# Kernel tuning notes

Measured on AMD Instinct MI355X. Metric: run time of the kernel, lower is better.

Reference implementation:

```python
import jax, jax.numpy as jnp
import numpy as np

DIM = 64
SQRT_DIM = np.sqrt(DIM).astype(np.float32)
NEG_INF = -1e9


def setup_inputs() -> dict:
    key = jax.random.key(0)
    kq, kk, kv, km = jax.random.split(key, 4)
    B, Q, K, D = 32, 1024, 1024, DIM
    query = jax.random.normal(kq, (B, Q, D), dtype=jnp.float32)
    k = jax.random.normal(kk, (B, K, D), dtype=jnp.float32)
    value = jax.random.normal(kv, (B, K, D), dtype=jnp.float32)
    mask = jax.random.randint(km, (B, Q, K), 0, 2).astype(jnp.bool_)
    return {"query": query, "key": k, "value": value, "mask": mask}


def reference(query, key, value, mask):
    # score: [B, Q, K]
    score = jnp.einsum('bqd,bkd->bqk', query, key) / SQRT_DIM
    score = jnp.where(mask, NEG_INF, score)
    attn = jax.nn.softmax(score, axis=-1)
    context = jnp.einsum('bqk,bkd->bqd', attn, value)
    return (context, attn)
```

## Files before the change

kernel.cpp:

```cpp
#include <hip/hip_runtime.h>

constexpr int BATCH = 32;
constexpr int QLEN  = 1024;
constexpr int KLEN  = 1024;
constexpr int DIM   = 64;
constexpr int TQ    = 16;

typedef float    f32x4 __attribute__((ext_vector_type(4)));
typedef int      i32x4 __attribute__((ext_vector_type(4)));
typedef _Float16 f16x8 __attribute__((ext_vector_type(8)));
typedef _Float16 f16x4 __attribute__((ext_vector_type(4)));
typedef unsigned long long u64;
typedef unsigned int u32;
typedef u64 u64x2 __attribute__((ext_vector_type(2)));

__device__ __forceinline__ f16x8 cvt_h8(f32x4 a, f32x4 b) {
  f16x8 h;
  h[0] = (_Float16)a[0]; h[1] = (_Float16)a[1]; h[2] = (_Float16)a[2]; h[3] = (_Float16)a[3];
  h[4] = (_Float16)b[0]; h[5] = (_Float16)b[1]; h[6] = (_Float16)b[2]; h[7] = (_Float16)b[3];
  return h;
}

constexpr int TK = 128;
__global__ __launch_bounds__(256)
void vtkh_kernel(const float* __restrict__ V, const float* __restrict__ Kg,
                 _Float16* __restrict__ Vt, _Float16* __restrict__ Kh) {
  __shared__ _Float16 lt[DIM][TK + 8];
  const int b = blockIdx.y, k0 = blockIdx.x * TK;
  const int t = threadIdx.x;
  const int d4 = (t & 15) * 4;
  #pragma unroll
  for (int p = 0; p < TK / 16; ++p) {
    const int kl = (t >> 4) + p * 16;
    const f32x4 v = *(const f32x4*)(V + ((size_t)(b * KLEN + k0 + kl)) * DIM + d4);
    #pragma unroll
    for (int j = 0; j < 4; ++j) lt[d4 + j][kl] = (_Float16)v[j];
  }
  #pragma unroll
  for (int p = 0; p < 8; ++p) {
    const int idx = t + p * 256;
    const int kl = idx >> 4, dd = (idx & 15) * 4;
    const f32x4 v = *(const f32x4*)(Kg + ((size_t)(b * KLEN + k0 + kl)) * DIM + dd);
    f16x4 h = { (_Float16)v[0], (_Float16)v[1], (_Float16)v[2], (_Float16)v[3] };
    *(f16x4*)(Kh + ((size_t)(b * KLEN + k0 + kl)) * DIM + dd) = h;
  }
  __syncthreads();
  const int d = t >> 2;
  #pragma unroll
  for (int j2 = 0; j2 < TK / 32; ++j2) {
    const int seg = (t & 3) + j2 * 4;
    *(f16x8*)(Vt + (size_t)b * DIM * KLEN + (size_t)d * KLEN + k0 + seg * 8) =
        *(const f16x8*)(&lt[d][seg * 8]);
  }
}

__global__ __launch_bounds__(256)
void maskpack_kernel(const int* __restrict__ Mg, u64* __restrict__ Mp) {
  const int l  = threadIdx.x & 63;
  const int gw = blockIdx.x * 4 + (threadIdx.x >> 6);
  for (int row = gw; row < BATCH * QLEN; row += 8192) {
    const int* mr = Mg + (size_t)row * KLEN;
    u64 myw = 0;
    #pragma unroll
    for (int c = 0; c < 4; ++c) {
      const i32x4 v = __builtin_nontemporal_load((const i32x4*)(mr + c * 256 + l * 4));
      #pragma unroll
      for (int u = 0; u < 4; ++u) {
        const u64 bl = __ballot(v[u] != 0);
        if (l == c * 4 + u) myw = bl;
      }
    }
    if (l < 16) Mp[(size_t)row * 16 + l] = myw;
  }
}

__global__ __launch_bounds__(64)
void sdpa_kernel(const float* __restrict__ Qg, const _Float16* __restrict__ Kh,
                 const _Float16* __restrict__ Vt, const u64* __restrict__ Mp,
                 float* __restrict__ Ctx, float* __restrict__ Attn)
{
  const int l    = threadIdx.x;
  const int n16  = l & 15;
  const int quad = l >> 4;

  const int lin  = blockIdx.x;
  const int nlin = (lin & 7) * (BATCH * (QLEN / TQ) / 8) + (lin >> 3);
  const int b    = nlin >> 6;
  const int q0   = (nlin & 63) * TQ;

  const float* qb = Qg + ((size_t)(b * QLEN + q0 + n16)) * DIM + quad * 8;
  f32x4 qa0 = *(const f32x4*)(qb),      qa1 = *(const f32x4*)(qb + 4);
  f32x4 qa2 = *(const f32x4*)(qb + 32), qa3 = *(const f32x4*)(qb + 36);
  #pragma unroll
  for (int i = 0; i < 4; ++i) { qa0[i] *= 0.125f; qa1[i] *= 0.125f; qa2[i] *= 0.125f; qa3[i] *= 0.125f; }
  const f16x8 aq0 = cvt_h8(qa0, qa1);
  const f16x8 aq1 = cvt_h8(qa2, qa3);

  const _Float16* kb_base = Kh + (size_t)b * KLEN * DIM + quad * 8;
  const u64* mrow = Mp + ((size_t)(b * QLEN + q0 + n16)) * 16;

  float rsum = 0.f;
  #pragma unroll
  for (int g = 0; g < 4; ++g) {
    const u64x2 w01 = *(const u64x2*)(mrow + g * 4);
    const u64x2 w23 = *(const u64x2*)(mrow + g * 4 + 2);
    const u64 w[4] = { w01[0], w01[1], w23[0], w23[1] };
    #pragma unroll
    for (int tt = 0; tt < 16; ++tt) {
      const int t = g * 16 + tt;
      const _Float16* kp = kb_base + (size_t)(t * 16 + n16) * DIM;
      const f16x8 ak0 = *(const f16x8*)(kp);
      const f16x8 ak1 = *(const f16x8*)(kp + 32);
      f32x4 acc = {0.f, 0.f, 0.f, 0.f};
      acc = __builtin_amdgcn_mfma_f32_16x16x32_f16(ak0, aq0, acc, 0, 0, 0);
      acc = __builtin_amdgcn_mfma_f32_16x16x32_f16(ak1, aq1, acc, 0, 0, 0);
      const u32 sh = tt * 4 + quad;
      #pragma unroll
      for (int i = 0; i < 4; ++i)
        rsum += ((w[i] >> sh) & 1ULL) ? 0.f : __expf(acc[i]);
    }
  }
  rsum += __shfl_xor(rsum, 16, 64);
  rsum += __shfl_xor(rsum, 32, 64);
  const float inv = __builtin_amdgcn_rcpf(rsum);

  float* arow = Attn + ((size_t)(b * QLEN + q0 + n16)) * KLEN;
  const _Float16* vtb = Vt + (size_t)b * DIM * KLEN;
  f32x4 cacc[4] = { {0.f,0.f,0.f,0.f}, {0.f,0.f,0.f,0.f}, {0.f,0.f,0.f,0.f}, {0.f,0.f,0.f,0.f} };
  #pragma unroll
  for (int g = 0; g < 4; ++g) {
    const u64x2 w01 = *(const u64x2*)(mrow + g * 4);
    const u64x2 w23 = *(const u64x2*)(mrow + g * 4 + 2);
    const u64 w[4] = { w01[0], w01[1], w23[0], w23[1] };
    #pragma unroll
    for (int m = 0; m < 8; ++m) {
      uint2 pw[2];
      #pragma unroll
      for (int h = 0; h < 2; ++h) {
        const int t = g * 16 + m * 2 + h;
        const _Float16* kp = kb_base + (size_t)(t * 16 + n16) * DIM;
        const f16x8 ak0 = *(const f16x8*)(kp);
        const f16x8 ak1 = *(const f16x8*)(kp + 32);
        f32x4 acc = {0.f, 0.f, 0.f, 0.f};
        acc = __builtin_amdgcn_mfma_f32_16x16x32_f16(ak0, aq0, acc, 0, 0, 0);
        acc = __builtin_amdgcn_mfma_f32_16x16x32_f16(ak1, aq1, acc, 0, 0, 0);
        const u32 sh = (t & 15) * 4 + quad;
        f32x4 e;
        #pragma unroll
        for (int i = 0; i < 4; ++i)
          e[i] = ((w[i] >> sh) & 1ULL) ? 0.f : __expf(acc[i]) * inv;
        *(f32x4*)(arow + t * 16 + quad * 4) = e;
        f16x4 ph = { (_Float16)e[0], (_Float16)e[1], (_Float16)e[2], (_Float16)e[3] };
        __builtin_memcpy(&pw[h], &ph, 8);
      }
      const int s0 = n16 + ((quad & 1) << 5);
      const u32 x0a = (u32)__shfl((int)pw[0].x, s0, 64);
      const u32 y0a = (u32)__shfl((int)pw[0].y, s0, 64);
      const u32 x1a = (u32)__shfl((int)pw[1].x, s0, 64);
      const u32 y1a = (u32)__shfl((int)pw[1].y, s0, 64);
      const u32 x0b = (u32)__shfl((int)pw[0].x, s0 + 16, 64);
      const u32 y0b = (u32)__shfl((int)pw[0].y, s0 + 16, 64);
      const u32 x1b = (u32)__shfl((int)pw[1].x, s0 + 16, 64);
      const u32 y1b = (u32)__shfl((int)pw[1].y, s0 + 16, 64);
      const bool hs = (quad & 2) != 0;
      const u32 dd[4] = { hs ? x1a : x0a, hs ? y1a : y0a,
                          hs ? x1b : x0b, hs ? y1b : y0b };
      f16x8 pa; __builtin_memcpy(&pa, dd, 16);
      const int K0 = g * 256 + m * 32;
      #pragma unroll
      for (int dt = 0; dt < 4; ++dt) {
        const f16x8 bv = *(const f16x8*)(vtb + (size_t)(dt * 16 + n16) * KLEN + K0 + quad * 8);
        cacc[dt] = __builtin_amdgcn_mfma_f32_16x16x32_f16(pa, bv, cacc[dt], 0, 0, 0);
      }
    }
  }
  #pragma unroll
  for (int dt = 0; dt < 4; ++dt)
    #pragma unroll
    for (int i = 0; i < 4; ++i)
      Ctx[((size_t)(b * QLEN + q0 + quad * 4 + i)) * DIM + dt * 16 + n16] = cacc[dt][i];
}

extern "C" void kernel_launch(void* const* d_in, const int* in_sizes, int n_in,
                              void* d_out, int out_size, void* d_ws, size_t ws_size,
                              hipStream_t stream) {
  const float* Qg = (const float*)d_in[0];
  const float* Kg = (const float*)d_in[1];
  const float* Vg = (const float*)d_in[2];
  const int*   Mg = (const int*)d_in[3];
  float* Ctx  = (float*)d_out;
  float* Attn = (float*)d_out + (size_t)BATCH * QLEN * DIM;
  _Float16* Vt = (_Float16*)d_ws;
  u64* Mp = (u64*)((char*)d_ws + (size_t)BATCH * DIM * KLEN * 2);
  _Float16* Kh = (_Float16*)((char*)d_ws + (size_t)BATCH * DIM * KLEN * 2 +
                             (size_t)BATCH * QLEN * 16 * 8);

  dim3 tgrid(KLEN / TK, BATCH);
  vtkh_kernel<<<tgrid, 256, 0, stream>>>(Vg, Kg, Vt, Kh);

  maskpack_kernel<<<2048, 256, 0, stream>>>(Mg, Mp);

  sdpa_kernel<<<2048, 64, 0, stream>>>(Qg, Kh, Vt, Mp, Ctx, Attn);
}
```

Before: 332.2 us.

## Fuse mask read into attention kernel and split key range across four waves

Removes the separate mask-packing kernel, so the attention kernel reads the int mask directly. Each block now has four waves, each handling a quarter of the keys. Row sums are combined through shared memory, and context partials are reduced in LDS before the store. Exponentials are cached as fp16 from the first pass, so QK is not recomputed, and exp2 with a log2e-folded scale replaces expf. The trade-off is more LDS use, two block barriers and fp16 rounding of the cached exponentials before the attention output is written.

```diff
diff --git a/kernel.cpp b/kernel.cpp
--- a/kernel.cpp
+++ b/kernel.cpp
@@ -12,7 +12,6 @@
 typedef _Float16 f16x4 __attribute__((ext_vector_type(4)));
 typedef unsigned long long u64;
 typedef unsigned int u32;
-typedef u64 u64x2 __attribute__((ext_vector_type(2)));
 
 __device__ __forceinline__ f16x8 cvt_h8(f32x4 a, f32x4 b) {
   f16x8 h;
@@ -54,32 +53,17 @@
   }
 }
 
-__global__ __launch_bounds__(256)
-void maskpack_kernel(const int* __restrict__ Mg, u64* __restrict__ Mp) {
-  const int l  = threadIdx.x & 63;
-  const int gw = blockIdx.x * 4 + (threadIdx.x >> 6);
-  for (int row = gw; row < BATCH * QLEN; row += 8192) {
-    const int* mr = Mg + (size_t)row * KLEN;
-    u64 myw = 0;
-    #pragma unroll
-    for (int c = 0; c < 4; ++c) {
-      const i32x4 v = __builtin_nontemporal_load((const i32x4*)(mr + c * 256 + l * 4));
-      #pragma unroll
-      for (int u = 0; u < 4; ++u) {
-        const u64 bl = __ballot(v[u] != 0);
-        if (l == c * 4 + u) myw = bl;
-      }
-    }
-    if (l < 16) Mp[(size_t)row * 16 + l] = myw;
-  }
-}
-
-__global__ __launch_bounds__(64)
+__global__ __launch_bounds__(256, 4)
 void sdpa_kernel(const float* __restrict__ Qg, const _Float16* __restrict__ Kh,
-                 const _Float16* __restrict__ Vt, const u64* __restrict__ Mp,
+                 const _Float16* __restrict__ Vt, const int* __restrict__ Mg,
                  float* __restrict__ Ctx, float* __restrict__ Attn)
 {
-  const int l    = threadIdx.x;
+  __shared__ float rs[4][16];
+  __shared__ float cx[4][16][65];
+
+  const int tid  = threadIdx.x;
+  const int w    = tid >> 6;
+  const int l    = tid & 63;
   const int n16  = l & 15;
   const int quad = l >> 4;
 
@@ -88,97 +72,94 @@
   const int b    = nlin >> 6;
   const int q0   = (nlin & 63) * TQ;
 
+  const float qscl = 0.125f * 1.44269504f;
   const float* qb = Qg + ((size_t)(b * QLEN + q0 + n16)) * DIM + quad * 8;
   f32x4 qa0 = *(const f32x4*)(qb),      qa1 = *(const f32x4*)(qb + 4);
   f32x4 qa2 = *(const f32x4*)(qb + 32), qa3 = *(const f32x4*)(qb + 36);
   #pragma unroll
-  for (int i = 0; i < 4; ++i) { qa0[i] *= 0.125f; qa1[i] *= 0.125f; qa2[i] *= 0.125f; qa3[i] *= 0.125f; }
+  for (int i = 0; i < 4; ++i) { qa0[i] *= qscl; qa1[i] *= qscl; qa2[i] *= qscl; qa3[i] *= qscl; }
   const f16x8 aq0 = cvt_h8(qa0, qa1);
   const f16x8 aq1 = cvt_h8(qa2, qa3);
 
-  const _Float16* kb_base = Kh + (size_t)b * KLEN * DIM + quad * 8;
-  const u64* mrow = Mp + ((size_t)(b * QLEN + q0 + n16)) * 16;
+  const _Float16* kb = Kh + (size_t)b * KLEN * DIM + quad * 8;
+  const int* mrow = Mg + ((size_t)(b * QLEN + q0 + n16)) * KLEN + w * 256 + quad * 4;
 
-  float rsum = 0.f;
+  f32x4 rsum4 = {0.f, 0.f, 0.f, 0.f};
+  f16x4 ec[16];
   #pragma unroll
-  for (int g = 0; g < 4; ++g) {
-    const u64x2 w01 = *(const u64x2*)(mrow + g * 4);
-    const u64x2 w23 = *(const u64x2*)(mrow + g * 4 + 2);
-    const u64 w[4] = { w01[0], w01[1], w23[0], w23[1] };
+  for (int tt = 0; tt < 16; ++tt) {
+    const i32x4 mv = *(const i32x4*)(mrow + tt * 16);
+    const _Float16* kp = kb + (size_t)((w * 16 + tt) * 16 + n16) * DIM;
+    const f16x8 ak0 = *(const f16x8*)(kp);
+    const f16x8 ak1 = *(const f16x8*)(kp + 32);
+    f32x4 acc = {0.f, 0.f, 0.f, 0.f};
+    acc = __builtin_amdgcn_mfma_f32_16x16x32_f16(ak0, aq0, acc, 0, 0, 0);
+    acc = __builtin_amdgcn_mfma_f32_16x16x32_f16(ak1, aq1, acc, 0, 0, 0);
+    f32x4 e;
     #pragma unroll
-    for (int tt = 0; tt < 16; ++tt) {
-      const int t = g * 16 + tt;
-      const _Float16* kp = kb_base + (size_t)(t * 16 + n16) * DIM;
-      const f16x8 ak0 = *(const f16x8*)(kp);
-      const f16x8 ak1 = *(const f16x8*)(kp + 32);
-      f32x4 acc = {0.f, 0.f, 0.f, 0.f};
-      acc = __builtin_amdgcn_mfma_f32_16x16x32_f16(ak0, aq0, acc, 0, 0, 0);
-      acc = __builtin_amdgcn_mfma_f32_16x16x32_f16(ak1, aq1, acc, 0, 0, 0);
-      const u32 sh = tt * 4 + quad;
-      #pragma unroll
-      for (int i = 0; i < 4; ++i)
-        rsum += ((w[i] >> sh) & 1ULL) ? 0.f : __expf(acc[i]);
+    for (int i = 0; i < 4; ++i) {
+      e[i] = mv[i] ? 0.f : __builtin_amdgcn_exp2f(acc[i]);
+      rsum4[i] += e[i];
     }
+    ec[tt] = f16x4{ (_Float16)e[0], (_Float16)e[1], (_Float16)e[2], (_Float16)e[3] };
   }
+  float rsum = (rsum4[0] + rsum4[1]) + (rsum4[2] + rsum4[3]);
   rsum += __shfl_xor(rsum, 16, 64);
   rsum += __shfl_xor(rsum, 32, 64);
-  const float inv = __builtin_amdgcn_rcpf(rsum);
+  if (quad == 0) rs[w][n16] = rsum;
+  __syncthreads();
+  const float inv =
+      __builtin_amdgcn_rcpf(rs[0][n16] + rs[1][n16] + rs[2][n16] + rs[3][n16]);
 
-  float* arow = Attn + ((size_t)(b * QLEN + q0 + n16)) * KLEN;
+  float* arow = Attn + ((size_t)(b * QLEN + q0 + n16)) * KLEN + w * 256;
   const _Float16* vtb = Vt + (size_t)b * DIM * KLEN;
   f32x4 cacc[4] = { {0.f,0.f,0.f,0.f}, {0.f,0.f,0.f,0.f}, {0.f,0.f,0.f,0.f}, {0.f,0.f,0.f,0.f} };
   #pragma unroll
-  for (int g = 0; g < 4; ++g) {
-    const u64x2 w01 = *(const u64x2*)(mrow + g * 4);
-    const u64x2 w23 = *(const u64x2*)(mrow + g * 4 + 2);
-    const u64 w[4] = { w01[0], w01[1], w23[0], w23[1] };
+  for (int m = 0; m < 8; ++m) {
+    uint2 pw[2];
     #pragma unroll
-    for (int m = 0; m < 8; ++m) {
-      uint2 pw[2];
+    for (int h = 0; h < 2; ++h) {
+      const int tt = m * 2 + h;
+      f32x4 ev;
       #pragma unroll
-      for (int h = 0; h < 2; ++h) {
-        const int t = g * 16 + m * 2 + h;
-        const _Float16* kp = kb_base + (size_t)(t * 16 + n16) * DIM;
-        const f16x8 ak0 = *(const f16x8*)(kp);
-        const f16x8 ak1 = *(const f16x8*)(kp + 32);
-        f32x4 acc = {0.f, 0.f, 0.f, 0.f};
-        acc = __builtin_amdgcn_mfma_f32_16x16x32_f16(ak0, aq0, acc, 0, 0, 0);
-        acc = __builtin_amdgcn_mfma_f32_16x16x32_f16(ak1, aq1, acc, 0, 0, 0);
-        const u32 sh = (t & 15) * 4 + quad;
-        f32x4 e;
-        #pragma unroll
-        for (int i = 0; i < 4; ++i)
-          e[i] = ((w[i] >> sh) & 1ULL) ? 0.f : __expf(acc[i]) * inv;
-        *(f32x4*)(arow + t * 16 + quad * 4) = e;
-        f16x4 ph = { (_Float16)e[0], (_Float16)e[1], (_Float16)e[2], (_Float16)e[3] };
-        __builtin_memcpy(&pw[h], &ph, 8);
-      }
-      const int s0 = n16 + ((quad & 1) << 5);
-      const u32 x0a = (u32)__shfl((int)pw[0].x, s0, 64);
-      const u32 y0a = (u32)__shfl((int)pw[0].y, s0, 64);
-      const u32 x1a = (u32)__shfl((int)pw[1].x, s0, 64);
-      const u32 y1a = (u32)__shfl((int)pw[1].y, s0, 64);
-      const u32 x0b = (u32)__shfl((int)pw[0].x, s0 + 16, 64);
-      const u32 y0b = (u32)__shfl((int)pw[0].y, s0 + 16, 64);
-      const u32 x1b = (u32)__shfl((int)pw[1].x, s0 + 16, 64);
-      const u32 y1b = (u32)__shfl((int)pw[1].y, s0 + 16, 64);
-      const bool hs = (quad & 2) != 0;
-      const u32 dd[4] = { hs ? x1a : x0a, hs ? y1a : y0a,
-                          hs ? x1b : x0b, hs ? y1b : y0b };
-      f16x8 pa; __builtin_memcpy(&pa, dd, 16);
-      const int K0 = g * 256 + m * 32;
-      #pragma unroll
-      for (int dt = 0; dt < 4; ++dt) {
-        const f16x8 bv = *(const f16x8*)(vtb + (size_t)(dt * 16 + n16) * KLEN + K0 + quad * 8);
-        cacc[dt] = __builtin_amdgcn_mfma_f32_16x16x32_f16(pa, bv, cacc[dt], 0, 0, 0);
-      }
+      for (int i = 0; i < 4; ++i) ev[i] = (float)ec[tt][i] * inv;
+      *(f32x4*)(arow + tt * 16 + quad * 4) = ev;
+      f16x4 ph = { (_Float16)ev[0], (_Float16)ev[1], (_Float16)ev[2], (_Float16)ev[3] };
+      __builtin_memcpy(&pw[h], &ph, 8);
+    }
+    const int s0 = n16 + ((quad & 1) << 5);
+    const u32 x0a = (u32)__shfl((int)pw[0].x, s0, 64);
+    const u32 y0a = (u32)__shfl((int)pw[0].y, s0, 64);
+    const u32 x1a = (u32)__shfl((int)pw[1].x, s0, 64);
+    const u32 y1a = (u32)__shfl((int)pw[1].y, s0, 64);
+    const u32 x0b = (u32)__shfl((int)pw[0].x, s0 + 16, 64);
+    const u32 y0b = (u32)__shfl((int)pw[0].y, s0 + 16, 64);
+    const u32 x1b = (u32)__shfl((int)pw[1].x, s0 + 16, 64);
+    const u32 y1b = (u32)__shfl((int)pw[1].y, s0 + 16, 64);
+    const bool hs = (quad & 2) != 0;
+    const u32 dd[4] = { hs ? x1a : x0a, hs ? y1a : y0a,
+                        hs ? x1b : x0b, hs ? y1b : y0b };
+    f16x8 pa; __builtin_memcpy(&pa, dd, 16);
+    const int K0 = w * 256 + m * 32;
+    #pragma unroll
+    for (int dt = 0; dt < 4; ++dt) {
+      const f16x8 bv = *(const f16x8*)(vtb + (size_t)(dt * 16 + n16) * KLEN + K0 + quad * 8);
+      cacc[dt] = __builtin_amdgcn_mfma_f32_16x16x32_f16(pa, bv, cacc[dt], 0, 0, 0);
     }
   }
+
   #pragma unroll
   for (int dt = 0; dt < 4; ++dt)
     #pragma unroll
     for (int i = 0; i < 4; ++i)
-      Ctx[((size_t)(b * QLEN + q0 + quad * 4 + i)) * DIM + dt * 16 + n16] = cacc[dt][i];
+      cx[w][quad * 4 + i][dt * 16 + n16] = cacc[dt][i];
+  __syncthreads();
+  #pragma unroll
+  for (int rr = 0; rr < 4; ++rr) {
+    const int row = w * 4 + rr;
+    const float v = (cx[0][row][l] + cx[1][row][l]) + (cx[2][row][l] + cx[3][row][l]);
+    Ctx[((size_t)(b * QLEN + q0 + row)) * DIM + l] = v;
+  }
 }
 
 extern "C" void kernel_launch(void* const* d_in, const int* in_sizes, int n_in,
@@ -191,14 +172,10 @@
   float* Ctx  = (float*)d_out;
   float* Attn = (float*)d_out + (size_t)BATCH * QLEN * DIM;
   _Float16* Vt = (_Float16*)d_ws;
-  u64* Mp = (u64*)((char*)d_ws + (size_t)BATCH * DIM * KLEN * 2);
-  _Float16* Kh = (_Float16*)((char*)d_ws + (size_t)BATCH * DIM * KLEN * 2 +
-                             (size_t)BATCH * QLEN * 16 * 8);
+  _Float16* Kh = (_Float16*)((char*)d_ws + (size_t)BATCH * DIM * KLEN * 2);
 
   dim3 tgrid(KLEN / TK, BATCH);
   vtkh_kernel<<<tgrid, 256, 0, stream>>>(Vg, Kg, Vt, Kh);
 
-  maskpack_kernel<<<2048, 256, 0, stream>>>(Mg, Mp);
-
-  sdpa_kernel<<<2048, 64, 0, stream>>>(Qg, Kh, Vt, Mp, Ctx, Attn);
+  sdpa_kernel<<<2048, 256, 0, stream>>>(Qg, Kh, Vt, Mg, Ctx, Attn);
 }
```

Measured after the change: 321.4 us. 3.3% less time.
